# Optimization experiments

Hardware: AMD Instinct MI355X
Metric: run time of the kernel (lower is better)

Reference implementation:

```python
import jax, jax.numpy as jnp
import numpy as np

EPS = 1e-07

def ternary_quantize(w, gamma=1.0):
    # gamma' = gamma / (mean|W| + eps)
    w_bar = jnp.mean(jnp.abs(w))
    gamma_prime = gamma / (w_bar + EPS)
    q = jnp.where(w > 0.5, 1.0, jnp.where(w < -0.5, -1.0, 0.0)).astype(w.dtype)
    # RoundClip(gamma' * q, -1, 1); jnp.round matches torch.round (half-to-even)
    return jnp.clip(jnp.round(gamma_prime * q), -1.0, 1.0)

def setup_inputs() -> dict:
    key = jax.random.key(0)
    kx, kw = jax.random.split(key)
    x = jax.random.normal(kx, (4, 2048, 4096), dtype=jnp.float32)
    weight = jax.random.normal(kw, (4096, 4096), dtype=jnp.float32)  # [out, in]
    return {"x": x, "weight": weight}

def reference(x, weight):
    wq = ternary_quantize(weight)
    # F.linear: x @ W^T
    return jnp.einsum('bsi,oi->bso', x, wq)
```

## Files before the change

kernel.cpp:

```cpp
#include <hip/hip_runtime.h>
#include <hip/hip_bf16.h>
#include <stdint.h>


typedef __bf16 bf16x8 __attribute__((ext_vector_type(8)));
typedef float  f32x4  __attribute__((ext_vector_type(4)));

#define EPS 1e-7f
#define NPART 4096

__device__ __forceinline__ void async_load16(const void* g, void* l) {
    __builtin_amdgcn_global_load_lds(
        (__attribute__((address_space(1))) void*)(const_cast<void*>(g)),
        (__attribute__((address_space(3))) void*)l,
        16, 0, 0);
}

__device__ __forceinline__ unsigned short f2bf_rne(float f) {
    unsigned u = __float_as_uint(f);
    unsigned r = (u + 0x7fffu + ((u >> 16) & 1u)) >> 16;
    return (unsigned short)r;
}

__device__ __forceinline__ float scale_from_partials(const float* __restrict__ partials,
                                                     float invCount) {
    const int lane = threadIdx.x & 63;
    const float4* p4 = (const float4*)partials;
    float s = 0.0f;
    #pragma unroll
    for (int j = 0; j < NPART / 4 / 64; ++j) {
        float4 v = p4[lane + 64 * j];
        s += v.x + v.y + v.z + v.w;
    }
    #pragma unroll
    for (int off = 32; off > 0; off >>= 1) s += __shfl_down(s, off, 64);
    s = __shfl(s, 0, 64);
    float mean = s * invCount;
    float gp = 1.0f / (mean + EPS);
    return fminf(fmaxf(rintf(gp), -1.0f), 1.0f);
}


__device__ __forceinline__ unsigned short tern_bf16(float w) {
    return (w > 0.5f) ? (unsigned short)0x3F80u
         : ((w < -0.5f) ? (unsigned short)0xBF80u : (unsigned short)0u);
}

__global__ __launch_bounds__(256) void quant_w_bf16(
    const float* __restrict__ in, ushort4* __restrict__ out,
    float* __restrict__ partials, int n4)
{
    int tid = blockIdx.x * blockDim.x + threadIdx.x;
    int stride = gridDim.x * blockDim.x;
    float s = 0.0f;
    for (int i = tid; i < n4; i += stride) {
        float4 v = ((const float4*)in)[i];
        s += fabsf(v.x) + fabsf(v.y) + fabsf(v.z) + fabsf(v.w);
        ushort4 r;
        r.x = tern_bf16(v.x); r.y = tern_bf16(v.y);
        r.z = tern_bf16(v.z); r.w = tern_bf16(v.w);
        out[i] = r;
    }
    #pragma unroll
    for (int off = 32; off > 0; off >>= 1) s += __shfl_down(s, off, 64);
    __shared__ float psum[4];
    int lane = threadIdx.x & 63, wid = threadIdx.x >> 6;
    if (lane == 0) psum[wid] = s;
    __syncthreads();
    if (threadIdx.x == 0)
        partials[blockIdx.x] = psum[0] + psum[1] + psum[2] + psum[3];
}


__global__ __launch_bounds__(256) void conv_x_bf16(
    const float* __restrict__ in, ushort4* __restrict__ out, int n4)
{
    int i = blockIdx.x * blockDim.x + threadIdx.x;
    if (i < n4) {
        float4 v = ((const float4*)in)[i];
        ushort4 r;
        r.x = f2bf_rne(v.x); r.y = f2bf_rne(v.y);
        r.z = f2bf_rne(v.z); r.w = f2bf_rne(v.w);
        out[i] = r;
    }
}


#define BM 128
#define BN 128
#define BK 64

__global__ __launch_bounds__(256) void gemm_bt(
    const __bf16* __restrict__ A,
    const __bf16* __restrict__ B,
    float* __restrict__ C,
    const float* __restrict__ partials,
    int N, int K, float invCount)
{
    __shared__ __bf16 As[BM * BK];
    __shared__ __bf16 Bs[BN * BK];

    const int t    = threadIdx.x;
    const int lane = t & 63;
    const int wid  = t >> 6;
    const int mBase = blockIdx.y * BM;
    const int nBase = blockIdx.x * BN;
    const int wm = (wid >> 1) * 64;
    const int wn = (wid & 1) * 64;
    const int lm = lane & 15;
    const int quad = lane >> 4;
    const int lm7 = lm & 7;

    f32x4 acc[4][4] = {};

    const __bf16* gA = A + (size_t)mBase * K;
    const __bf16* gB = B + (size_t)nBase * K;

    for (int k0 = 0; k0 < K; k0 += BK) {
        #pragma unroll
        for (int i = 0; i < 4; ++i) {
            int ch = i * 256 + t;
            int row = ch >> 3, sc = ch & 7;
            int cc = sc ^ (row & 7);
            async_load16(gA + (size_t)row * K + k0 + cc * 8, &As[ch * 8]);
        }
        #pragma unroll
        for (int i = 0; i < 4; ++i) {
            int ch = i * 256 + t;
            int row = ch >> 3, sc = ch & 7;
            int cc = sc ^ (row & 7);
            async_load16(gB + (size_t)row * K + k0 + cc * 8, &Bs[ch * 8]);
        }
        __syncthreads();

        #pragma unroll
        for (int ks = 0; ks < BK; ks += 32) {
            const int cc = (ks >> 3) + quad;
            const int swz = cc ^ lm7;
            bf16x8 af[4], bfr[4];
            #pragma unroll
            for (int mt = 0; mt < 4; ++mt)
                af[mt] = *(const bf16x8*)&As[((wm + mt * 16 + lm) * 8 + swz) * 8];
            #pragma unroll
            for (int nt = 0; nt < 4; ++nt)
                bfr[nt] = *(const bf16x8*)&Bs[((wn + nt * 16 + lm) * 8 + swz) * 8];
            #pragma unroll
            for (int mt = 0; mt < 4; ++mt)
                #pragma unroll
                for (int nt = 0; nt < 4; ++nt)
                    acc[mt][nt] = __builtin_amdgcn_mfma_f32_16x16x32_bf16(
                        af[mt], bfr[nt], acc[mt][nt], 0, 0, 0);
        }
        __syncthreads();
    }

    const float tscale = scale_from_partials(partials, invCount);

    #pragma unroll
    for (int mt = 0; mt < 4; ++mt) {
        #pragma unroll
        for (int nt = 0; nt < 4; ++nt) {
            #pragma unroll
            for (int r = 0; r < 4; ++r) {
                int row = mBase + wm + mt * 16 + quad * 4 + r;
                int col = nBase + wn + nt * 16 + lm;
                C[(size_t)row * N + col] = tscale * acc[mt][nt][r];
            }
        }
    }
}


__global__ void gemm_fallback(const float* __restrict__ x, const float* __restrict__ w,
                              float* __restrict__ out, const float* __restrict__ partials,
                              int N, int K, float invCount)
{
    __shared__ float xs[16][17];
    __shared__ float qs[16][17];
    int tx = threadIdx.x & 15;
    int ty = threadIdx.x >> 4;
    int row = blockIdx.y * 16 + ty;
    int col = blockIdx.x * 16 + tx;
    float acc = 0.0f;
    for (int k0 = 0; k0 < K; k0 += 16) {
        xs[ty][tx] = x[(size_t)row * K + k0 + tx];
        float wv = w[(size_t)(blockIdx.x * 16 + ty) * K + k0 + tx];
        qs[ty][tx] = (wv > 0.5f) ? 1.0f : ((wv < -0.5f) ? -1.0f : 0.0f);
        __syncthreads();
        #pragma unroll
        for (int j = 0; j < 16; ++j) acc += xs[ty][j] * qs[tx][j];
        __syncthreads();
    }
    float tscale = scale_from_partials(partials, invCount);
    out[(size_t)row * N + col] = tscale * acc;
}

__global__ __launch_bounds__(256) void absmean_only(
    const float* __restrict__ w, float* __restrict__ partials, int n4)
{
    int tid = blockIdx.x * blockDim.x + threadIdx.x;
    int stride = gridDim.x * blockDim.x;
    float s = 0.0f;
    for (int i = tid; i < n4; i += stride) {
        float4 v = ((const float4*)w)[i];
        s += fabsf(v.x) + fabsf(v.y) + fabsf(v.z) + fabsf(v.w);
    }
    #pragma unroll
    for (int off = 32; off > 0; off >>= 1) s += __shfl_down(s, off, 64);
    __shared__ float psum[4];
    int lane = threadIdx.x & 63, wid = threadIdx.x >> 6;
    if (lane == 0) psum[wid] = s;
    __syncthreads();
    if (threadIdx.x == 0)
        partials[blockIdx.x] = psum[0] + psum[1] + psum[2] + psum[3];
}


extern "C" void kernel_launch(void* const* d_in, const int* in_sizes, int n_in,
                              void* d_out, int out_size, void* d_ws, size_t ws_size,
                              hipStream_t stream) {
    const float* x = (const float*)d_in[0];
    const float* w = (const float*)d_in[1];
    float* out = (float*)d_out;

    const int K = 4096;
    const int M = in_sizes[0] / K;
    const int N = in_sizes[1] / K;
    const float invCount = 1.0f / (float)(in_sizes[1]);

    float* partials = (float*)d_ws;
    const size_t base = NPART * sizeof(float);
    const size_t need = base + (size_t)M * K * 2 + (size_t)N * K * 2;

    if (ws_size >= need) {
        __bf16* xb = (__bf16*)((char*)d_ws + base);
        __bf16* qb = (__bf16*)((char*)d_ws + base + (size_t)M * K * 2);

        int xn4 = (M * K) / 4;
        int wn4 = (N * K) / 4;
        quant_w_bf16<<<NPART, 256, 0, stream>>>(w, (ushort4*)qb, partials, wn4);
        conv_x_bf16<<<(xn4 + 255) / 256, 256, 0, stream>>>(x, (ushort4*)xb, xn4);

        dim3 grid(N / BN, M / BM);
        gemm_bt<<<grid, 256, 0, stream>>>(xb, qb, out, partials, N, K, invCount);
    } else {
        absmean_only<<<NPART, 256, 0, stream>>>(w, partials, in_sizes[1] / 4);
        dim3 grid(N / 16, M / 16);
        gemm_fallback<<<grid, 256, 0, stream>>>(x, w, out, partials, N, K, invCount);
    }
}
```

Before: 571.9 us.

## Rewrite bf16 GEMM as 256x256 tile, 8-wave, double-buffered pipelined kernel

The GEMM moves from a 128x128x64 tile with 4 waves and a single LDS buffer to a 256x256x32 tile with 8 waves. LDS is double-buffered, and the A and B global-to-LDS loads are staggered so they overlap with the MFMA halves. It also adds s_setprio around the MFMA bursts, a new XOR swizzle, and a workgroup-ID remap across the 8 XCDs for L2 locality. This targets exposed load latency and global traffic, at the cost of more registers (128 accumulator floats per lane) and a more fragile barrier and waitcnt schedule.

```diff
diff --git a/kernel.cpp b/kernel.cpp
--- a/kernel.cpp
+++ b/kernel.cpp
@@ -86,84 +86,113 @@
 }
 
 
-#define BM 128
-#define BN 128
-#define BK 64
-
-__global__ __launch_bounds__(256) void gemm_bt(
+#define BM 256
+#define BN 256
+#define BK 32
+
+#define GEMM_TILE(t_, CUR, NXT)                                                \
+  {                                                                            \
+    const int tA = ((t_) + 1 < T) ? ((t_) + 1) : (t_);                         \
+    const int tB = ((t_) + 2 < T) ? ((t_) + 2) : (t_);                         \
+    bf16x8 a[8], b[4];                                                         \
+    _Pragma("unroll")                                                          \
+    for (int mt = 0; mt < 8; ++mt)                                             \
+      a[mt] = *(const bf16x8*)&As[CUR][wr][(mt * 16 + lm) * BK + slot8];       \
+    _Pragma("unroll")                                                          \
+    for (int nt = 0; nt < 4; ++nt)                                             \
+      b[nt] = *(const bf16x8*)&Bs[CUR][wh][(wb + nt * 16 + lm) * BK + slot8];  \
+    async_load16(gA + (size_t)tA * BK,        &As[NXT][0][(size_t)tid * 8]);   \
+    async_load16(gA + gH1 + (size_t)tA * BK,  &As[NXT][1][(size_t)tid * 8]);   \
+    __builtin_amdgcn_s_barrier();                                              \
+    asm volatile("s_waitcnt lgkmcnt(0)" ::: "memory");                         \
+    __builtin_amdgcn_s_setprio(1);                                             \
+    _Pragma("unroll")                                                          \
+    for (int mt = 0; mt < 8; ++mt) {                                           \
+      acc[mt][0] = __builtin_amdgcn_mfma_f32_16x16x32_bf16(a[mt], b[0], acc[mt][0], 0, 0, 0); \
+      acc[mt][1] = __builtin_amdgcn_mfma_f32_16x16x32_bf16(a[mt], b[1], acc[mt][1], 0, 0, 0); \
+    }                                                                          \
+    __builtin_amdgcn_s_setprio(0);                                             \
+    __builtin_amdgcn_s_barrier();                                              \
+    async_load16(gB + (size_t)tB * BK,        &Bs[CUR][0][(size_t)tid * 8]);   \
+    async_load16(gB + gH1 + (size_t)tB * BK,  &Bs[CUR][1][(size_t)tid * 8]);   \
+    __builtin_amdgcn_s_barrier();                                              \
+    __builtin_amdgcn_s_setprio(1);                                             \
+    _Pragma("unroll")                                                          \
+    for (int mt = 0; mt < 8; ++mt) {                                           \
+      acc[mt][2] = __builtin_amdgcn_mfma_f32_16x16x32_bf16(a[mt], b[2], acc[mt][2], 0, 0, 0); \
+      acc[mt][3] = __builtin_amdgcn_mfma_f32_16x16x32_bf16(a[mt], b[3], acc[mt][3], 0, 0, 0); \
+    }                                                                          \
+    __builtin_amdgcn_s_setprio(0);                                             \
+    asm volatile("s_waitcnt vmcnt(2)" ::: "memory");                           \
+    __builtin_amdgcn_s_barrier();                                              \
+  }
+
+__global__ __launch_bounds__(512, 2) void gemm_bt(
     const __bf16* __restrict__ A,
     const __bf16* __restrict__ B,
     float* __restrict__ C,
     const float* __restrict__ partials,
     int N, int K, float invCount)
 {
-    __shared__ __bf16 As[BM * BK];
-    __shared__ __bf16 Bs[BN * BK];
-
-    const int t    = threadIdx.x;
-    const int lane = t & 63;
-    const int wid  = t >> 6;
-    const int mBase = blockIdx.y * BM;
-    const int nBase = blockIdx.x * BN;
-    const int wm = (wid >> 1) * 64;
-    const int wn = (wid & 1) * 64;
-    const int lm = lane & 15;
+    __shared__ __bf16 As[2][2][128 * BK];
+    __shared__ __bf16 Bs[2][2][128 * BK];
+
+    const int tid  = threadIdx.x;
+    const int lane = tid & 63;
+    const int wid  = tid >> 6;
+    const int wr   = wid >> 2;
+    const int wc   = wid & 3;
+    const int wh   = wc >> 1;
+    const int wb   = (wc & 1) * 64;
+    const int lm   = lane & 15;
     const int quad = lane >> 4;
-    const int lm7 = lm & 7;
-
-    f32x4 acc[4][4] = {};
-
-    const __bf16* gA = A + (size_t)mBase * K;
-    const __bf16* gB = B + (size_t)nBase * K;
-
-    for (int k0 = 0; k0 < K; k0 += BK) {
-        #pragma unroll
-        for (int i = 0; i < 4; ++i) {
-            int ch = i * 256 + t;
-            int row = ch >> 3, sc = ch & 7;
-            int cc = sc ^ (row & 7);
-            async_load16(gA + (size_t)row * K + k0 + cc * 8, &As[ch * 8]);
-        }
-        #pragma unroll
-        for (int i = 0; i < 4; ++i) {
-            int ch = i * 256 + t;
-            int row = ch >> 3, sc = ch & 7;
-            int cc = sc ^ (row & 7);
-            async_load16(gB + (size_t)row * K + k0 + cc * 8, &Bs[ch * 8]);
-        }
-        __syncthreads();
-
-        #pragma unroll
-        for (int ks = 0; ks < BK; ks += 32) {
-            const int cc = (ks >> 3) + quad;
-            const int swz = cc ^ lm7;
-            bf16x8 af[4], bfr[4];
-            #pragma unroll
-            for (int mt = 0; mt < 4; ++mt)
-                af[mt] = *(const bf16x8*)&As[((wm + mt * 16 + lm) * 8 + swz) * 8];
-            #pragma unroll
-            for (int nt = 0; nt < 4; ++nt)
-                bfr[nt] = *(const bf16x8*)&Bs[((wn + nt * 16 + lm) * 8 + swz) * 8];
-            #pragma unroll
-            for (int mt = 0; mt < 4; ++mt)
-                #pragma unroll
-                for (int nt = 0; nt < 4; ++nt)
-                    acc[mt][nt] = __builtin_amdgcn_mfma_f32_16x16x32_bf16(
-                        af[mt], bfr[nt], acc[mt][nt], 0, 0, 0);
-        }
-        __syncthreads();
-    }
+
+    const int gx  = gridDim.x;
+    const int nwg = gx * gridDim.y;
+    int wg = blockIdx.y * gx + blockIdx.x;
+    wg = (wg & 7) * (nwg >> 3) + (wg >> 3);
+    const int mBase = (wg / gx) * BM;
+    const int nBase = (wg % gx) * BN;
+
+    const int srow = tid >> 2;
+    const int scc  = (tid & 3) ^ (srow & 3) ^ ((srow >> 2) & 3);
+    const int slot8 = (quad ^ (lm & 3) ^ ((lm >> 2) & 3)) * 8;
+
+    const __bf16* gA = A + (size_t)(mBase + srow) * K + scc * 8;
+    const __bf16* gB = B + (size_t)(nBase + srow) * K + scc * 8;
+    const size_t gH1 = (size_t)128 * K;
+
+    const int T = K / BK;
+    f32x4 acc[8][4] = {};
+
+    {
+        const size_t k1 = (T > 1) ? BK : 0;
+        async_load16(gB,            &Bs[0][0][(size_t)tid * 8]);
+        async_load16(gB + gH1,      &Bs[0][1][(size_t)tid * 8]);
+        async_load16(gA,            &As[0][0][(size_t)tid * 8]);
+        async_load16(gA + gH1,      &As[0][1][(size_t)tid * 8]);
+        async_load16(gB + k1,       &Bs[1][0][(size_t)tid * 8]);
+        async_load16(gB + gH1 + k1, &Bs[1][1][(size_t)tid * 8]);
+    }
+    asm volatile("s_waitcnt vmcnt(2)" ::: "memory");
+    __builtin_amdgcn_s_barrier();
+
+    for (int t = 0; t < T; t += 2) {
+        GEMM_TILE(t,     0, 1);
+        GEMM_TILE(t + 1, 1, 0);
+    }
+    asm volatile("s_waitcnt vmcnt(0)" ::: "memory");
 
     const float tscale = scale_from_partials(partials, invCount);
 
     #pragma unroll
-    for (int mt = 0; mt < 4; ++mt) {
+    for (int mt = 0; mt < 8; ++mt) {
         #pragma unroll
         for (int nt = 0; nt < 4; ++nt) {
             #pragma unroll
             for (int r = 0; r < 4; ++r) {
-                int row = mBase + wm + mt * 16 + quad * 4 + r;
-                int col = nBase + wn + nt * 16 + lm;
+                int row = mBase + wr * 128 + mt * 16 + quad * 4 + r;
+                int col = nBase + wc * 64 + nt * 16 + lm;
                 C[(size_t)row * N + col] = tscale * acc[mt][nt][r];
             }
         }
@@ -232,7 +261,9 @@
     const size_t base = NPART * sizeof(float);
     const size_t need = base + (size_t)M * K * 2 + (size_t)N * K * 2;
 
-    if (ws_size >= need) {
+    const bool shapes_ok = (M % BM == 0) && (N % BN == 0) && (K % (2 * BK) == 0);
+
+    if (ws_size >= need && shapes_ok) {
         __bf16* xb = (__bf16*)((char*)d_ws + base);
         __bf16* qb = (__bf16*)((char*)d_ws + base + (size_t)M * K * 2);
 
@@ -242,7 +273,7 @@
         conv_x_bf16<<<(xn4 + 255) / 256, 256, 0, stream>>>(x, (ushort4*)xb, xn4);
 
         dim3 grid(N / BN, M / BM);
-        gemm_bt<<<grid, 256, 0, stream>>>(xb, qb, out, partials, N, K, invCount);
+        gemm_bt<<<grid, 512, 0, stream>>>(xb, qb, out, partials, N, K, invCount);
     } else {
         absmean_only<<<NPART, 256, 0, stream>>>(w, partials, in_sizes[1] / 4);
         dim3 grid(N / 16, M / 16);
```

Measured after the change: 524.3 us. 1.09x faster.
